# Kernel optimization log

Measured on AMD Instinct MI355X. Metric: run time of the kernel, lower is better.

The kernel has to match this reference:

```python
import jax, jax.numpy as jnp
import numpy as np

RANK = 8
LN_EPS = 1e-5


def setup_inputs() -> dict:
    key = jax.random.key(0)
    ks = jax.random.split(key, 8)
    B, T, D = 16, 1024, 1024
    A = 1024          # ada_dim
    I = 1024          # inter_dim
    OUT = D * RANK * 4  # 32768
    s = 0.02
    return {
        "x": jax.random.normal(ks[0], (B, T, D), jnp.float32),
        "ada_emb": jax.random.normal(ks[1], (B, A), jnp.float32),
        "base_up": jax.random.normal(ks[2], (D, D), jnp.float32) * s,
        "base_down": jax.random.normal(ks[3], (D, D), jnp.float32) * s,
        "ln_gamma": jnp.ones((A,), jnp.float32),
        "ln_beta": jnp.zeros((A,), jnp.float32),
        "W1": jax.random.normal(ks[4], (A, I), jnp.float32) / np.sqrt(A),
        "bias1": jnp.zeros((I,), jnp.float32),
        "W2": jax.random.normal(ks[5], (I, OUT), jnp.float32) / np.sqrt(I),
        "bias2": jnp.zeros((OUT,), jnp.float32),
    }


def reference(x, ada_emb, base_up, base_down, ln_gamma, ln_beta, W1, bias1, W2, bias2):
    B, T, D = x.shape
    R = RANK
    # norm_cond: LayerNorm over ada_dim (biased variance, eps=1e-5)
    mu = jnp.mean(ada_emb, axis=-1, keepdims=True)
    var = jnp.mean(jnp.square(ada_emb - mu), axis=-1, keepdims=True)
    c = (ada_emb - mu) / jnp.sqrt(var + LN_EPS) * ln_gamma + ln_beta
    # gen_weight: Linear -> GELU -> Linear
    h = jax.nn.gelu(c @ W1 + bias1, approximate=False)
    w = h @ W2 + bias2                         # (B, 4*D*R)
    a1, b1, a2, b2 = [t.reshape(B, D, R) for t in jnp.split(w, 4, axis=-1)]
    # down matvec: x @ (base_down + a2 @ b2^T), factored to avoid (B,D,D)
    u = jnp.einsum('btd,bdr->btr', x, a2)      # (B,T,R)
    mid = jnp.einsum('btd,dl->btl', x, base_down) + jnp.einsum('btr,blr->btl', u, b2)
    mid = jax.nn.gelu(mid, approximate=False)  # act_fn between layers
    # up matvec: (base_up + a1 @ b1^T) @ mid, factored
    v = jnp.einsum('blr,btl->btr', b1, mid)    # (B,T,R)
    out = jnp.einsum('btl,kl->btk', mid, base_up) + jnp.einsum('bkr,btr->btk', a1, v)
    return x + out  # residual
```

## Files before the change

### kernel.cpp

```cpp
#include <hip/hip_runtime.h>
#include <math.h>

#define DD 1024
#define NB 16
#define WSPLIT 16
#define HSPLIT 32

typedef unsigned short u16;
typedef __attribute__((ext_vector_type(8))) short short8;
typedef __attribute__((ext_vector_type(4))) float f32x4;
typedef __attribute__((ext_vector_type(16))) float f32x16;

__device__ __forceinline__ float gelu_f(float x) {
  return 0.5f * x * (1.0f + erff(x * 0.70710678118654752440f));
}
__device__ __forceinline__ u16 f2bf(float f) {
  union { float f; unsigned u; } v; v.f = f;
  return (u16)((v.u + 0x7FFFu + ((v.u >> 16) & 1u)) >> 16);
}
__device__ __forceinline__ float bf2f(u16 b) {
  union { unsigned u; float f; } v; v.u = ((unsigned)b) << 16;
  return v.f;
}
__device__ __forceinline__ void gload_lds16(const u16* g, u16* l) {
  __builtin_amdgcn_global_load_lds(
      (const __attribute__((address_space(1))) void*)g,
      (__attribute__((address_space(3))) void*)l, 16, 0, 0);
}
__device__ __forceinline__ void gload_lds16f(const float* g, float* l) {
  __builtin_amdgcn_global_load_lds(
      (const __attribute__((address_space(1))) void*)g,
      (__attribute__((address_space(3))) void*)l, 16, 0, 0);
}

#define VMCNT8   asm volatile("s_waitcnt vmcnt(8)" ::: "memory")
#define VMCNT0   asm volatile("s_waitcnt vmcnt(0)" ::: "memory")
#define BARRIER  asm volatile("s_barrier" ::: "memory")

__launch_bounds__(256)
__global__ void prep_kernel(const float* __restrict__ x, u16* __restrict__ xb,
                            const float* __restrict__ ada, const float* __restrict__ gamma,
                            const float* __restrict__ beta, float* __restrict__ c,
                            const float* __restrict__ bdn, u16* __restrict__ bdTb,
                            const float* __restrict__ bu, u16* __restrict__ bub) {
  __shared__ float smem[1056];
  int bid = blockIdx.x;
  int t = threadIdx.x;
  if (bid < 8192) {
    size_t i = (size_t)bid * 256 + t;
    const float4* xf = (const float4*)x;
    float4 v0 = xf[i * 2], v1 = xf[i * 2 + 1];
    short8 o;
    o[0] = (short)f2bf(v0.x); o[1] = (short)f2bf(v0.y);
    o[2] = (short)f2bf(v0.z); o[3] = (short)f2bf(v0.w);
    o[4] = (short)f2bf(v1.x); o[5] = (short)f2bf(v1.y);
    o[6] = (short)f2bf(v1.z); o[7] = (short)f2bf(v1.w);
    *(short8*)(xb + i * 8) = o;
  } else if (bid < 8208) {
    int b = bid - 8192;
    const float* row = ada + b * DD;
    float s = 0.f, s2 = 0.f;
    for (int i = t; i < DD; i += 256) { float v = row[i]; s += v; s2 += v * v; }
    for (int off = 32; off; off >>= 1) { s += __shfl_down(s, off); s2 += __shfl_down(s2, off); }
    float* rs = smem; float* rs2 = smem + 4;
    int wave = t >> 6, lane = t & 63;
    if (lane == 0) { rs[wave] = s; rs2[wave] = s2; }
    __syncthreads();
    if (t == 0) {
      float a = 0.f, a2 = 0.f;
      for (int w = 0; w < 4; w++) { a += rs[w]; a2 += rs2[w]; }
      rs[0] = a * (1.0f / DD); rs2[0] = a2 * (1.0f / DD);
    }
    __syncthreads();
    float mu = rs[0];
    float var = rs2[0] - mu * mu;
    float inv = rsqrtf(var + 1e-5f);
    for (int i = t; i < DD; i += 256)
      c[b * DD + i] = (row[i] - mu) * inv * gamma[i] + beta[i];
  } else if (bid < 9232) {
    int t2 = bid - 8208;
    int bx = (t2 & 31) * 32, by = (t2 >> 5) * 32;
    float (*tile)[33] = (float(*)[33])smem;
    int tx = t & 31, ty = t >> 5;
    for (int r = ty; r < 32; r += 8) tile[r][tx] = bdn[(size_t)(by + r) * DD + bx + tx];
    __syncthreads();
    for (int r = ty; r < 32; r += 8)
      bdTb[(size_t)(bx + r) * DD + by + tx] = f2bf(tile[tx][r]);
  } else {
    size_t i = (size_t)(bid - 9232) * 256 + t;
    const float4* bf = (const float4*)bu;
    float4 v0 = bf[i * 2], v1 = bf[i * 2 + 1];
    short8 o;
    o[0] = (short)f2bf(v0.x); o[1] = (short)f2bf(v0.y);
    o[2] = (short)f2bf(v0.z); o[3] = (short)f2bf(v0.w);
    o[4] = (short)f2bf(v1.x); o[5] = (short)f2bf(v1.y);
    o[6] = (short)f2bf(v1.z); o[7] = (short)f2bf(v1.w);
    *(short8*)(bub + i * 8) = o;
  }
}

__launch_bounds__(256)
__global__ void h_part_kernel(const float* __restrict__ c, const float* __restrict__ W1,
                              float* __restrict__ hpart) {
  int s = blockIdx.y;
  int j = blockIdx.x * 256 + threadIdx.x;
  int k0 = s * 32;
  __shared__ float cs[NB][32];
  for (int i = threadIdx.x; i < NB * 32; i += 256)
    cs[i >> 5][i & 31] = c[(size_t)(i >> 5) * DD + k0 + (i & 31)];
  __syncthreads();
  float acc[NB];
  #pragma unroll
  for (int b = 0; b < NB; b++) acc[b] = 0.f;
  #pragma unroll
  for (int al = 0; al < 32; al++) {
    float wv = W1[(size_t)(k0 + al) * DD + j];
    #pragma unroll
    for (int b = 0; b < NB; b++) acc[b] += cs[b][al] * wv;
  }
  #pragma unroll
  for (int b = 0; b < NB; b++)
    hpart[((size_t)s * NB + b) * DD + j] = acc[b];
}

__launch_bounds__(256)
__global__ void h_reduce_kernel(const float* __restrict__ hpart, const float* __restrict__ bias1,
                                float* __restrict__ h) {
  int idx = blockIdx.x * 256 + threadIdx.x;
  int j = idx & (DD - 1);
  float acc = bias1[j];
  #pragma unroll
  for (int s = 0; s < HSPLIT; s++) acc += hpart[(size_t)s * NB * DD + idx];
  h[idx] = gelu_f(acc);
}

#define WSTAGE(I8, BUF) do { int kr_ = k0 + (I8) * 8;                                \
    _Pragma("unroll")                                                                \
    for (int r_ = 0; r_ < 8; r_++)                                                   \
      gload_lds16f(W2 + (size_t)(kr_ + r_) * 32768 + j0 + t4, &wlds[BUF][r_][t4]);   \
  } while (0)

__launch_bounds__(256)
__global__ void w_part_kernel(const float* __restrict__ h, const float* __restrict__ W2,
                              float* __restrict__ part) {
  int s = blockIdx.y;
  int j0 = blockIdx.x * 1024;
  int k0 = s * 64;
  int t = threadIdx.x;
  int t4 = t * 4;
  __shared__ __align__(16) float wlds[2][8][1024];
  __shared__ __align__(16) float hlT[64][16];

  float hv[4];
  #pragma unroll
  for (int v = 0; v < 4; v++) {
    int i = t + v * 256;
    hv[v] = h[(size_t)(i & 15) * DD + k0 + (i >> 4)];
  }
  #pragma unroll
  for (int v = 0; v < 4; v++) {
    int i = t + v * 256;
    hlT[i >> 4][i & 15] = hv[v];
  }

  WSTAGE(0, 0);
  WSTAGE(1, 1);

  f32x4 acc[NB];
  #pragma unroll
  for (int b = 0; b < NB; b++) acc[b] = f32x4{0.f, 0.f, 0.f, 0.f};

  #pragma unroll 1
  for (int i8 = 0; i8 < 8; i8++) {
    if (i8 < 7) { VMCNT8; } else { VMCNT0; }
    BARRIER;
    int buf = i8 & 1;
    #pragma unroll
    for (int r = 0; r < 8; r++) {
      f32x4 wv = *(const f32x4*)&wlds[buf][r][t4];
      int kk = i8 * 8 + r;
      f32x4 hx0 = *(const f32x4*)&hlT[kk][0];
      f32x4 hx1 = *(const f32x4*)&hlT[kk][4];
      f32x4 hx2 = *(const f32x4*)&hlT[kk][8];
      f32x4 hx3 = *(const f32x4*)&hlT[kk][12];
      #pragma unroll
      for (int q = 0; q < 4; q++) {
        acc[q][0] += hx0[q] * wv[0]; acc[q][1] += hx0[q] * wv[1];
        acc[q][2] += hx0[q] * wv[2]; acc[q][3] += hx0[q] * wv[3];
        acc[q + 4][0] += hx1[q] * wv[0]; acc[q + 4][1] += hx1[q] * wv[1];
        acc[q + 4][2] += hx1[q] * wv[2]; acc[q + 4][3] += hx1[q] * wv[3];
        acc[q + 8][0] += hx2[q] * wv[0]; acc[q + 8][1] += hx2[q] * wv[1];
        acc[q + 8][2] += hx2[q] * wv[2]; acc[q + 8][3] += hx2[q] * wv[3];
        acc[q + 12][0] += hx3[q] * wv[0]; acc[q + 12][1] += hx3[q] * wv[1];
        acc[q + 12][2] += hx3[q] * wv[2]; acc[q + 12][3] += hx3[q] * wv[3];
      }
    }
    BARRIER;
    if (i8 + 2 < 8) WSTAGE(i8 + 2, buf);
  }

  int j4 = blockIdx.x * 256 + t;
  f32x4* pv = (f32x4*)part;
  #pragma unroll
  for (int b = 0; b < NB; b++)
    pv[((size_t)s * NB + b) * 8192 + j4] = acc[b];
}

__launch_bounds__(256)
__global__ void w_reduce_kernel(const float* __restrict__ part, const float* __restrict__ bias2,
                                float* __restrict__ w) {
  int idx = blockIdx.x * 256 + threadIdx.x;
  int j = idx & 32767;
  float acc = bias2[j];
  #pragma unroll
  for (int s = 0; s < WSPLIT; s++) acc += part[(size_t)s * NB * 32768 + idx];
  w[idx] = acc;
}

__launch_bounds__(256)
__global__ void pack_lora_kernel(const u16* __restrict__ src, const float* __restrict__ w,
                                 int aoff, int boff,
                                 u16* __restrict__ aext, u16* __restrict__ bext) {
  int b = blockIdx.y;
  const float* wb = w + (size_t)b * 32768;
  int t = threadIdx.x;
  short8 z = {};
  if (blockIdx.x < 16) {
    __shared__ float a2s[8192];
    for (int i = t; i < 8192; i += 256) a2s[i] = wb[aoff + i];
    __syncthreads();
    int row = blockIdx.x * 64 + (t >> 2);
    int q = t & 3;
    const u16* xr = src + ((size_t)b << 20) + (size_t)row * DD + q * 256;
    float acc[8] = {};
    #pragma unroll 4
    for (int kk = 0; kk < 32; kk++) {
      short8 xv = *(const short8*)(xr + kk * 8);
      #pragma unroll
      for (int e = 0; e < 8; e++) {
        float xf = bf2f((u16)xv[e]);
        int d = q * 256 + kk * 8 + e;
        #pragma unroll
        for (int r = 0; r < 8; r++) acc[r] += xf * a2s[d * 8 + r];
      }
    }
    #pragma unroll
    for (int r = 0; r < 8; r++) {
      acc[r] += __shfl_xor(acc[r], 1);
      acc[r] += __shfl_xor(acc[r], 2);
    }
    short8 ov = z;
    if (q == 0) {
      #pragma unroll
      for (int r = 0; r < 8; r++) ov[r] = (short)f2bf(acc[r]);
    }
    u16* orow = aext + ((size_t)b * 1024 + row) * 64 + q * 16;
    *(short8*)orow = ov;
    *(short8*)(orow + 8) = z;
  } else {
    for (int l = t; l < 1024; l += 256) {
      short8 ov;
      #pragma unroll
      for (int r = 0; r < 8; r++) ov[r] = (short)f2bf(wb[boff + l * 8 + r]);
      u16* orow = bext + ((size_t)b * 1024 + l) * 64;
      *(short8*)orow = ov;
      #pragma unroll
      for (int k = 1; k < 8; k++) *(short8*)(orow + k * 8) = z;
    }
  }
}

#define STAGE_A(KT, BUF) do { int kt_ = (KT);                                          \
    if (kt_ < 16) { int ks_ = kt_ * 64;                                                \
      _Pragma("unroll")                                                                \
      for (int c_ = 0; c_ < 4; c_++)                                                   \
        gload_lds16(Ab + (size_t)srow[c_] * DD + ks_ + se[c_], As[BUF] + ldsel[c_]);   \
    } else {                                                                           \
      _Pragma("unroll")                                                                \
      for (int c_ = 0; c_ < 4; c_++)                                                   \
        gload_lds16(Ae + (size_t)srow[c_] * 64 + se[c_], As[BUF] + ldsel[c_]);         \
    } } while (0)
#define STAGE_B(KT, BUF) do { int kt_ = (KT);                                          \
    if (kt_ < 16) { int ks_ = kt_ * 64;                                                \
      _Pragma("unroll")                                                                \
      for (int c_ = 0; c_ < 4; c_++)                                                   \
        gload_lds16(Bb + (size_t)srow[c_] * DD + ks_ + se[c_], Bs[BUF] + ldsel[c_]);   \
    } else {                                                                           \
      _Pragma("unroll")                                                                \
      for (int c_ = 0; c_ < 4; c_++)                                                   \
        gload_lds16(Be + (size_t)srow[c_] * 64 + se[c_], Bs[BUF] + ldsel[c_]);         \
    } } while (0)

template<int PHASE>
__launch_bounds__(512, 2)
__global__ void gemm256_kernel(const u16* __restrict__ A, const u16* __restrict__ BT,
                               const u16* __restrict__ Aext, const u16* __restrict__ Bext,
                               const u16* __restrict__ resid, void* __restrict__ Cout) {
  constexpr int BK = 64;
  constexpr int NT = 17;
  __shared__ __align__(16) u16 As[2][256 * BK];
  __shared__ __align__(16) u16 Bs[2][256 * BK];

  int orig = blockIdx.x;
  int logical = (orig & 7) * 32 + (orig >> 3);
  int b = logical >> 4;
  int tile = logical & 15;
  int tm = tile >> 2, tn = tile & 3;

  const u16* Ab = A + ((size_t)b << 20) + (size_t)(tm * 256) * DD;
  const u16* Bb = BT + (size_t)(tn * 256) * DD;
  const u16* Ae = Aext + ((size_t)b * 1024 + tm * 256) * 64;
  const u16* Be = Bext + ((size_t)b * 1024 + tn * 256) * 64;

  int t = threadIdx.x, lane = t & 63;
  int l31 = lane & 31, kb = (lane >> 5) * 8;
  int wave = t >> 6;
  int wm = wave >> 2, wn = wave & 3;

  int srow[4], se[4], ldsel[4];
  #pragma unroll
  for (int c = 0; c < 4; c++) {
    int chunk = c * 512 + t;
    srow[c] = chunk >> 3;
    se[c] = ((chunk & 7) ^ (srow[c] & 7)) << 3;
    ldsel[c] = chunk * 8;
  }

  f32x16 acc[4][2] = {};

  STAGE_A(0, 0); STAGE_B(0, 0);
  STAGE_A(1, 1); STAGE_B(1, 1);
  VMCNT8;
  BARRIER;

  int cur = 0;
  #pragma unroll 1
  for (int kt = 0; kt < NT; kt++) {
    const u16* Ap = As[cur];
    const u16* Bp = Bs[cur];
    short8 afr[2][4], bf0[4], bf1[4];

    #pragma unroll
    for (int ks = 0; ks < 4; ks++) {
      #pragma unroll
      for (int rt = 0; rt < 2; rt++) {
        int r = wm * 128 + rt * 32 + l31;
        int e = (ks * 16 + kb) ^ ((r & 7) << 3);
        afr[rt][ks] = *(const short8*)(Ap + r * BK + e);
      }
      {
        int r = wn * 64 + l31;
        int e = (ks * 16 + kb) ^ ((r & 7) << 3);
        bf0[ks] = *(const short8*)(Bp + r * BK + e);
      }
    }
    BARRIER;
    __builtin_amdgcn_s_setprio(1);
    #pragma unroll
    for (int ks = 0; ks < 4; ks++)
      #pragma unroll
      for (int rt = 0; rt < 2; rt++)
        acc[rt][0] = __builtin_amdgcn_mfma_f32_32x32x16_bf16(afr[rt][ks], bf0[ks], acc[rt][0], 0, 0, 0);
    __builtin_amdgcn_s_setprio(0);
    BARRIER;

    #pragma unroll
    for (int ks = 0; ks < 4; ks++) {
      int r = wn * 64 + 32 + l31;
      int e = (ks * 16 + kb) ^ ((r & 7) << 3);
      bf1[ks] = *(const short8*)(Bp + r * BK + e);
    }
    BARRIER;
    __builtin_amdgcn_s_setprio(1);
    #pragma unroll
    for (int ks = 0; ks < 4; ks++)
      #pragma unroll
      for (int rt = 0; rt < 2; rt++)
        acc[rt][1] = __builtin_amdgcn_mfma_f32_32x32x16_bf16(afr[rt][ks], bf1[ks], acc[rt][1], 0, 0, 0);
    __builtin_amdgcn_s_setprio(0);
    BARRIER;

    if (kt + 2 < NT) STAGE_B(kt + 2, cur);
    #pragma unroll
    for (int ks = 0; ks < 4; ks++)
      #pragma unroll
      for (int rt = 0; rt < 2; rt++) {
        int r = wm * 128 + (rt + 2) * 32 + l31;
        int e = (ks * 16 + kb) ^ ((r & 7) << 3);
        afr[rt][ks] = *(const short8*)(Ap + r * BK + e);
      }
    BARRIER;
    __builtin_amdgcn_s_setprio(1);
    #pragma unroll
    for (int ks = 0; ks < 4; ks++)
      #pragma unroll
      for (int rt = 0; rt < 2; rt++)
        acc[rt + 2][1] = __builtin_amdgcn_mfma_f32_32x32x16_bf16(afr[rt][ks], bf1[ks], acc[rt + 2][1], 0, 0, 0);
    __builtin_amdgcn_s_setprio(0);
    BARRIER;

    if (kt + 2 < NT) STAGE_A(kt + 2, cur);
    __builtin_amdgcn_s_setprio(1);
    #pragma unroll
    for (int ks = 0; ks < 4; ks++)
      #pragma unroll
      for (int rt = 0; rt < 2; rt++)
        acc[rt + 2][0] = __builtin_amdgcn_mfma_f32_32x32x16_bf16(afr[rt][ks], bf0[ks], acc[rt + 2][0], 0, 0, 0);
    __builtin_amdgcn_s_setprio(0);
    if (kt + 2 < NT) { VMCNT8; } else { VMCNT0; }
    BARRIER;

    cur ^= 1;
  }

  int r0 = tm * 256 + wm * 128 + (lane >> 5) * 4;
  int c0 = tn * 256 + wn * 64 + l31;
  if (PHASE == 1) {
    u16* mid = (u16*)Cout + ((size_t)b << 20);
    #pragma unroll
    for (int rt = 0; rt < 4; rt++)
      #pragma unroll
      for (int ct = 0; ct < 2; ct++)
        #pragma unroll
        for (int reg = 0; reg < 16; reg++) {
          int row = r0 + rt * 32 + (reg & 3) + 8 * (reg >> 2);
          int col = c0 + ct * 32;
          mid[(size_t)row * DD + col] = f2bf(gelu_f(acc[rt][ct][reg]));
        }
  } else {
    float* out = (float*)Cout + ((size_t)b << 20);
    const u16* xb = resid + ((size_t)b << 20);
    #pragma unroll
    for (int rt = 0; rt < 4; rt++)
      #pragma unroll
      for (int ct = 0; ct < 2; ct++)
        #pragma unroll
        for (int reg = 0; reg < 16; reg++) {
          int row = r0 + rt * 32 + (reg & 3) + 8 * (reg >> 2);
          int col = c0 + ct * 32;
          size_t idx = (size_t)row * DD + col;
          out[idx] = bf2f(xb[idx]) + acc[rt][ct][reg];
        }
  }
}

extern "C" void kernel_launch(void* const* d_in, const int* in_sizes, int n_in,
                              void* d_out, int out_size, void* d_ws, size_t ws_size,
                              hipStream_t stream) {
  const float* x         = (const float*)d_in[0];
  const float* ada       = (const float*)d_in[1];
  const float* base_up   = (const float*)d_in[2];
  const float* base_down = (const float*)d_in[3];
  const float* gamma     = (const float*)d_in[4];
  const float* beta      = (const float*)d_in[5];
  const float* W1        = (const float*)d_in[6];
  const float* bias1     = (const float*)d_in[7];
  const float* W2        = (const float*)d_in[8];
  const float* bias2     = (const float*)d_in[9];
  float* out = (float*)d_out;
  char* ws = (char*)d_ws;

  float* c     = (float*)(ws);
  float* h     = (float*)(ws + 0x10000);
  float* w     = (float*)(ws + 0x20000);
  u16*   bdTb  = (u16*)  (ws + 0x220000);
  u16*   bub   = (u16*)  (ws + 0x420000);
  float* hpart = (float*)(ws + 0x620000);
  u16*   xb    = (u16*)  (ws + 0x820000);
  u16*   uext  = (u16*)  (ws + 0x2820000);
  u16*   b2ext = (u16*)  (ws + 0x2A20000);
  u16*   vext  = (u16*)  (ws + 0x2C20000);
  u16*   a1ext = (u16*)  (ws + 0x2E20000);
  u16*   mid   = (u16*)  (ws + 0x3020000);
  float* part  = (float*)(ws + 0x5020000);

  prep_kernel<<<dim3(9744), dim3(256), 0, stream>>>(x, xb, ada, gamma, beta, c,
                                                    base_down, bdTb, base_up, bub);
  h_part_kernel<<<dim3(4, HSPLIT), dim3(256), 0, stream>>>(c, W1, hpart);
  h_reduce_kernel<<<dim3(64), dim3(256), 0, stream>>>(hpart, bias1, h);
  w_part_kernel<<<dim3(32, WSPLIT), dim3(256), 0, stream>>>(h, W2, part);
  w_reduce_kernel<<<dim3(2048), dim3(256), 0, stream>>>(part, bias2, w);
  pack_lora_kernel<<<dim3(17, 16), dim3(256), 0, stream>>>(xb, w, 16384, 24576, uext, b2ext);
  gemm256_kernel<1><<<dim3(256), dim3(512), 0, stream>>>(xb, bdTb, uext, b2ext,
                                                         (const u16*)nullptr, (void*)mid);
  pack_lora_kernel<<<dim3(17, 16), dim3(256), 0, stream>>>(mid, w, 8192, 0, vext, a1ext);
  gemm256_kernel<2><<<dim3(256), dim3(512), 0, stream>>>(mid, bub, vext, a1ext, xb, (void*)out);
}
```

Baseline: 258.1 us.

## Retile W2 generation kernel and drop intra-iteration barriers in main GEMM

The W2 partial-product kernel is retiled: each block now covers 256 output columns over a 256-deep K slice (split-K reduced from 16 to 4), with one column per thread and 16-row stages. This shrinks the partial-sum buffer that w_reduce reads and writes. Separately, the bf16 GEMM loop drops the barriers between MFMA groups and issues both next-tile loads together after a single barrier. That cuts synchronisation overhead but gives up the finer load/compute interleaving. The per-thread FMA density in w_part also falls, since each LDS read now feeds only 16 FMAs instead of 64.

Result: no change. 254.6 us (-1.4%).

```diff
diff --git a/kernel.cpp b/kernel.cpp
--- a/kernel.cpp
+++ b/kernel.cpp
@@ -3,7 +3,7 @@
 
 #define DD 1024
 #define NB 16
-#define WSPLIT 16
+#define WSPLIT 4
 #define HSPLIT 32
 
 typedef unsigned short u16;
@@ -34,6 +34,7 @@
 }
 
 #define VMCNT8   asm volatile("s_waitcnt vmcnt(8)" ::: "memory")
+#define VMCNT4   asm volatile("s_waitcnt vmcnt(4)" ::: "memory")
 #define VMCNT0   asm volatile("s_waitcnt vmcnt(0)" ::: "memory")
 #define BARRIER  asm volatile("s_barrier" ::: "memory")
 
@@ -134,76 +135,62 @@
   h[idx] = gelu_f(acc);
 }
 
-#define WSTAGE(I8, BUF) do { int kr_ = k0 + (I8) * 8;                                \
-    _Pragma("unroll")                                                                \
-    for (int r_ = 0; r_ < 8; r_++)                                                   \
-      gload_lds16f(W2 + (size_t)(kr_ + r_) * 32768 + j0 + t4, &wlds[BUF][r_][t4]);   \
+#define WSTAGE(ST, BUF) do { int kr_ = k0 + (ST) * 16;                                      \
+    _Pragma("unroll")                                                                       \
+    for (int i_ = 0; i_ < 4; i_++)                                                          \
+      gload_lds16f(W2 + (size_t)(kr_ + i_ * 4 + (t >> 6)) * 32768 + j0 + ((t & 63) << 2),   \
+                   &wlds[BUF][i_ * 4 + (t >> 6)][(t & 63) << 2]);                           \
   } while (0)
 
 __launch_bounds__(256)
 __global__ void w_part_kernel(const float* __restrict__ h, const float* __restrict__ W2,
                               float* __restrict__ part) {
   int s = blockIdx.y;
-  int j0 = blockIdx.x * 1024;
-  int k0 = s * 64;
+  int j0 = blockIdx.x * 256;
+  int k0 = s * 256;
   int t = threadIdx.x;
-  int t4 = t * 4;
-  __shared__ __align__(16) float wlds[2][8][1024];
-  __shared__ __align__(16) float hlT[64][16];
-
-  float hv[4];
-  #pragma unroll
-  for (int v = 0; v < 4; v++) {
+  __shared__ __align__(16) float wlds[2][16][256];
+  __shared__ __align__(16) float hlT[256][20];
+
+  #pragma unroll
+  for (int v = 0; v < 16; v++) {
     int i = t + v * 256;
-    hv[v] = h[(size_t)(i & 15) * DD + k0 + (i >> 4)];
-  }
-  #pragma unroll
-  for (int v = 0; v < 4; v++) {
-    int i = t + v * 256;
-    hlT[i >> 4][i & 15] = hv[v];
+    hlT[i & 255][i >> 8] = h[(size_t)(i >> 8) * DD + k0 + (i & 255)];
   }
 
   WSTAGE(0, 0);
   WSTAGE(1, 1);
 
-  f32x4 acc[NB];
-  #pragma unroll
-  for (int b = 0; b < NB; b++) acc[b] = f32x4{0.f, 0.f, 0.f, 0.f};
+  float acc[NB] = {};
 
   #pragma unroll 1
-  for (int i8 = 0; i8 < 8; i8++) {
-    if (i8 < 7) { VMCNT8; } else { VMCNT0; }
+  for (int st = 0; st < 16; st++) {
+    if (st < 15) { VMCNT4; } else { VMCNT0; }
     BARRIER;
-    int buf = i8 & 1;
-    #pragma unroll
-    for (int r = 0; r < 8; r++) {
-      f32x4 wv = *(const f32x4*)&wlds[buf][r][t4];
-      int kk = i8 * 8 + r;
-      f32x4 hx0 = *(const f32x4*)&hlT[kk][0];
-      f32x4 hx1 = *(const f32x4*)&hlT[kk][4];
-      f32x4 hx2 = *(const f32x4*)&hlT[kk][8];
-      f32x4 hx3 = *(const f32x4*)&hlT[kk][12];
+    int buf = st & 1;
+    #pragma unroll
+    for (int r = 0; r < 16; r++) {
+      float wv = wlds[buf][r][t];
+      int kk = st * 16 + r;
+      f32x4 h0 = *(const f32x4*)&hlT[kk][0];
+      f32x4 h1 = *(const f32x4*)&hlT[kk][4];
+      f32x4 h2 = *(const f32x4*)&hlT[kk][8];
+      f32x4 h3 = *(const f32x4*)&hlT[kk][12];
       #pragma unroll
       for (int q = 0; q < 4; q++) {
-        acc[q][0] += hx0[q] * wv[0]; acc[q][1] += hx0[q] * wv[1];
-        acc[q][2] += hx0[q] * wv[2]; acc[q][3] += hx0[q] * wv[3];
-        acc[q + 4][0] += hx1[q] * wv[0]; acc[q + 4][1] += hx1[q] * wv[1];
-        acc[q + 4][2] += hx1[q] * wv[2]; acc[q + 4][3] += hx1[q] * wv[3];
-        acc[q + 8][0] += hx2[q] * wv[0]; acc[q + 8][1] += hx2[q] * wv[1];
-        acc[q + 8][2] += hx2[q] * wv[2]; acc[q + 8][3] += hx2[q] * wv[3];
-        acc[q + 12][0] += hx3[q] * wv[0]; acc[q + 12][1] += hx3[q] * wv[1];
-        acc[q + 12][2] += hx3[q] * wv[2]; acc[q + 12][3] += hx3[q] * wv[3];
+        acc[q]      += h0[q] * wv;
+        acc[q + 4]  += h1[q] * wv;
+        acc[q + 8]  += h2[q] * wv;
+        acc[q + 12] += h3[q] * wv;
       }
     }
     BARRIER;
-    if (i8 + 2 < 8) WSTAGE(i8 + 2, buf);
-  }
-
-  int j4 = blockIdx.x * 256 + t;
-  f32x4* pv = (f32x4*)part;
+    if (st + 2 < 16) WSTAGE(st + 2, buf);
+  }
+
   #pragma unroll
   for (int b = 0; b < NB; b++)
-    pv[((size_t)s * NB + b) * 8192 + j4] = acc[b];
+    part[((size_t)s * NB + b) * 32768 + j0 + t] = acc[b];
 }
 
 __launch_bounds__(256)
@@ -354,7 +341,6 @@
         bf0[ks] = *(const short8*)(Bp + r * BK + e);
       }
     }
-    BARRIER;
     __builtin_amdgcn_s_setprio(1);
     #pragma unroll
     for (int ks = 0; ks < 4; ks++)
@@ -362,7 +348,6 @@
       for (int rt = 0; rt < 2; rt++)
         acc[rt][0] = __builtin_amdgcn_mfma_f32_32x32x16_bf16(afr[rt][ks], bf0[ks], acc[rt][0], 0, 0, 0);
     __builtin_amdgcn_s_setprio(0);
-    BARRIER;
 
     #pragma unroll
     for (int ks = 0; ks < 4; ks++) {
@@ -370,7 +355,6 @@
       int e = (ks * 16 + kb) ^ ((r & 7) << 3);
       bf1[ks] = *(const short8*)(Bp + r * BK + e);
     }
-    BARRIER;
     __builtin_amdgcn_s_setprio(1);
     #pragma unroll
     for (int ks = 0; ks < 4; ks++)
@@ -378,9 +362,7 @@
       for (int rt = 0; rt < 2; rt++)
         acc[rt][1] = __builtin_amdgcn_mfma_f32_32x32x16_bf16(afr[rt][ks], bf1[ks], acc[rt][1], 0, 0, 0);
     __builtin_amdgcn_s_setprio(0);
-    BARRIER;
-
-    if (kt + 2 < NT) STAGE_B(kt + 2, cur);
+
     #pragma unroll
     for (int ks = 0; ks < 4; ks++)
       #pragma unroll
@@ -389,25 +371,28 @@
         int e = (ks * 16 + kb) ^ ((r & 7) << 3);
         afr[rt][ks] = *(const short8*)(Ap + r * BK + e);
       }
-    BARRIER;
     __builtin_amdgcn_s_setprio(1);
     #pragma unroll
     for (int ks = 0; ks < 4; ks++)
       #pragma unroll
       for (int rt = 0; rt < 2; rt++)
         acc[rt + 2][1] = __builtin_amdgcn_mfma_f32_32x32x16_bf16(afr[rt][ks], bf1[ks], acc[rt + 2][1], 0, 0, 0);
-    __builtin_amdgcn_s_setprio(0);
-    BARRIER;
-
-    if (kt + 2 < NT) STAGE_A(kt + 2, cur);
-    __builtin_amdgcn_s_setprio(1);
+
     #pragma unroll
     for (int ks = 0; ks < 4; ks++)
       #pragma unroll
       for (int rt = 0; rt < 2; rt++)
         acc[rt + 2][0] = __builtin_amdgcn_mfma_f32_32x32x16_bf16(afr[rt][ks], bf0[ks], acc[rt + 2][0], 0, 0, 0);
     __builtin_amdgcn_s_setprio(0);
-    if (kt + 2 < NT) { VMCNT8; } else { VMCNT0; }
+
+    BARRIER;
+    if (kt + 2 < NT) {
+      STAGE_B(kt + 2, cur);
+      STAGE_A(kt + 2, cur);
+      VMCNT8;
+    } else {
+      VMCNT0;
+    }
     BARRIER;
 
     cur ^= 1;
@@ -478,7 +463,7 @@
                                                     base_down, bdTb, base_up, bub);
   h_part_kernel<<<dim3(4, HSPLIT), dim3(256), 0, stream>>>(c, W1, hpart);
   h_reduce_kernel<<<dim3(64), dim3(256), 0, stream>>>(hpart, bias1, h);
-  w_part_kernel<<<dim3(32, WSPLIT), dim3(256), 0, stream>>>(h, W2, part);
+  w_part_kernel<<<dim3(128, WSPLIT), dim3(256), 0, stream>>>(h, W2, part);
   w_reduce_kernel<<<dim3(2048), dim3(256), 0, stream>>>(part, bias2, w);
   pack_lora_kernel<<<dim3(17, 16), dim3(256), 0, stream>>>(xb, w, 16384, 24576, uext, b2ext);
   gemm256_kernel<1><<<dim3(256), dim3(512), 0, stream>>>(xb, bdTb, uext, b2ext,
```
